# Kernel tuning notes

Hardware: AMD Instinct MI355X
Metric: run time of the kernel (lower is better)

## Reference

```python
import jax, jax.numpy as jnp
import numpy as np

TEMPERATURE = 0.5


def setup_inputs() -> dict:
    key = jax.random.key(0)
    k1, k2 = jax.random.split(key)
    N, Z = 4096, 2048
    z1 = jax.random.normal(k1, (N, Z), dtype=jnp.float32)
    z2 = jax.random.normal(k2, (N, Z), dtype=jnp.float32)
    return {"z1": z1, "z2": z2}


def reference(z1, z2):
    # NT-Xent loss. Original torch code: normalize, build full 2Nx2N cosine-sim
    # matrix, prepend the positive pair column, cross-entropy with label 0.
    # Mathematically, per-row CE with the positive prepended and the self-sim
    # removed equals: logsumexp over the row excluding the diagonal, minus the
    # positive logit.  (cosine_similarity on already-normalized vectors is a
    # plain dot product, so normalization is applied once.)
    n, _ = z1.shape
    a = z1 / jnp.linalg.norm(z1, axis=1, keepdims=True)  # [N, Z]
    b = z2 / jnp.linalg.norm(z2, axis=1, keepdims=True)  # [N, Z]
    reps = jnp.concatenate([a, b], axis=0)               # [2N, Z]
    logits = jnp.matmul(reps, reps.T) / TEMPERATURE      # [2N, 2N]
    NEG_INF = jnp.float32(-1e9)  # mask self-similarity (excluded from CE denom)
    logits = jnp.where(jnp.eye(2 * n, dtype=bool), NEG_INF, logits)
    pos = jnp.sum(a * b, axis=1) / TEMPERATURE           # [N] positive logits
    pos = jnp.concatenate([pos, pos])                    # [2N]
    lse = jax.nn.logsumexp(logits, axis=1)               # [2N]
    # sum of CE over 2N rows, divided by 2N  == mean
    return jnp.mean(lse - pos)
```

## Files before the change

kernel.cpp:

```cpp
#include <hip/hip_runtime.h>
#include <stdint.h>

#define N_ROWS 4096
#define Z_DIM  2048
#define TOT    8192
#define TILE   128
#define RBYTES (Z_DIM / 2)
#define BKE    128
#define KBYT   (BKE / 2)
#define NITER  (Z_DIM / BKE)
#define NT     (TOT / TILE)
#define NBLK   (NT * (NT + 1) / 2)
#define INV_T  2.0f
#define SCL4   64.0f

typedef __attribute__((ext_vector_type(4))) int   intx4;
typedef __attribute__((ext_vector_type(8))) int   intx8;
typedef __attribute__((ext_vector_type(4))) float floatx4;

#define GLOAD16(g, l)                                                   \
    __builtin_amdgcn_global_load_lds(                                   \
        (const __attribute__((address_space(1))) unsigned int*)(g),     \
        (__attribute__((address_space(3))) unsigned int*)(l), 16, 0, 0)

__device__ __forceinline__ unsigned int f2fp4(float v) {
    float a = fabsf(v);
    unsigned int c = (a >= 0.25f) + (a >= 0.75f) + (a >= 1.25f) + (a >= 1.75f)
                   + (a >= 2.5f)  + (a >= 3.5f)  + (a >= 5.0f);
    return c | (v < 0.f ? 8u : 0u);
}

__global__ __launch_bounds__(256) void normalize_kernel(
    const float* __restrict__ z1, const float* __restrict__ z2,
    unsigned char* __restrict__ reps, float* __restrict__ pos,
    float* __restrict__ rowsum)
{
    const int row  = blockIdx.x;
    const int tid  = threadIdx.x;
    const int lane = tid & 63, wave = tid >> 6;

    if (row < TOT / 256) rowsum[row * 256 + tid] = 0.f;

    const float4* p1 = (const float4*)(z1 + (size_t)row * Z_DIM);
    const float4* p2 = (const float4*)(z2 + (size_t)row * Z_DIM);
    float4 x0 = p1[tid * 2], x1 = p1[tid * 2 + 1];
    float4 y0 = p2[tid * 2], y1 = p2[tid * 2 + 1];

    float s1 = x0.x*x0.x + x0.y*x0.y + x0.z*x0.z + x0.w*x0.w
             + x1.x*x1.x + x1.y*x1.y + x1.z*x1.z + x1.w*x1.w;
    float s2 = y0.x*y0.x + y0.y*y0.y + y0.z*y0.z + y0.w*y0.w
             + y1.x*y1.x + y1.y*y1.y + y1.z*y1.z + y1.w*y1.w;
    float dd = x0.x*y0.x + x0.y*y0.y + x0.z*y0.z + x0.w*y0.w
             + x1.x*y1.x + x1.y*y1.y + x1.z*y1.z + x1.w*y1.w;

    #pragma unroll
    for (int m = 1; m < 64; m <<= 1) {
        s1 += __shfl_xor(s1, m);
        s2 += __shfl_xor(s2, m);
        dd += __shfl_xor(dd, m);
    }
    __shared__ float red[3][4];
    if (lane == 0) { red[0][wave] = s1; red[1][wave] = s2; red[2][wave] = dd; }
    __syncthreads();
    s1 = red[0][0] + red[0][1] + red[0][2] + red[0][3];
    s2 = red[1][0] + red[1][1] + red[1][2] + red[1][3];
    dd = red[2][0] + red[2][1] + red[2][2] + red[2][3];

    const float inv1 = rsqrtf(s1), inv2 = rsqrtf(s2);
    if (tid == 0) {
        float p = dd * inv1 * inv2 * INV_T;
        pos[row] = p;
        pos[row + N_ROWS] = p;
    }

    const float a = inv1 * SCL4, b = inv2 * SCL4;
    unsigned int pa =  f2fp4(x0.x * a)        | (f2fp4(x0.y * a) << 4)
                    | (f2fp4(x0.z * a) << 8)  | (f2fp4(x0.w * a) << 12)
                    | (f2fp4(x1.x * a) << 16) | (f2fp4(x1.y * a) << 20)
                    | (f2fp4(x1.z * a) << 24) | (f2fp4(x1.w * a) << 28);
    unsigned int pb =  f2fp4(y0.x * b)        | (f2fp4(y0.y * b) << 4)
                    | (f2fp4(y0.z * b) << 8)  | (f2fp4(y0.w * b) << 12)
                    | (f2fp4(y1.x * b) << 16) | (f2fp4(y1.y * b) << 20)
                    | (f2fp4(y1.z * b) << 24) | (f2fp4(y1.w * b) << 28);
    *(unsigned int*)(reps + (size_t)row * RBYTES + tid * 4) = pa;
    *(unsigned int*)(reps + (size_t)(N_ROWS + row) * RBYTES + tid * 4) = pb;
}

__global__ __launch_bounds__(256) void simclr_gemm(
    const unsigned char* __restrict__ reps, float* __restrict__ rowsum)
{
    __shared__ __align__(16) unsigned char L[2][2][TILE * KBYT];

    const int t = blockIdx.x;
    int r = (int)((sqrtf(8.0f * (float)t + 1.0f) - 1.0f) * 0.5f);
    while ((r + 1) * (r + 2) / 2 <= t) ++r;
    while (r * (r + 1) / 2 > t) --r;
    const int bi = t - r * (r + 1) / 2;
    const int bj = r;
    const bool diag = (bi == bj);

    const int tid  = threadIdx.x;
    const int lane = tid & 63, wave = tid >> 6;
    const int wr = wave >> 1, wc = wave & 1;
    const int quad = lane >> 4, l16 = lane & 15;
    const int sw   = l16 & 3;
    const int row0 = bi * TILE, col0 = bj * TILE;

    floatx4 acc[4][4];
    #pragma unroll
    for (int i = 0; i < 4; ++i)
        #pragma unroll
        for (int j = 0; j < 4; ++j)
            acc[i][j] = floatx4{0.f, 0.f, 0.f, 0.f};

    const int c0 = tid, c1 = tid + 256;
    const int r0s = c0 >> 2, k0s = (c0 & 3) ^ (r0s & 3);
    const int r1s = c1 >> 2, k1s = (c1 & 3) ^ (r1s & 3);
    const unsigned char* gA0 = reps + (size_t)(row0 + r0s) * RBYTES + k0s * 16;
    const unsigned char* gA1 = reps + (size_t)(row0 + r1s) * RBYTES + k1s * 16;
    const unsigned char* gB0 = reps + (size_t)(col0 + r0s) * RBYTES + k0s * 16;
    const unsigned char* gB1 = reps + (size_t)(col0 + r1s) * RBYTES + k1s * 16;
    const int o0 = c0 * 16, o1 = c1 * 16;

    GLOAD16(gA0, &L[0][0][o0]);
    GLOAD16(gA1, &L[0][0][o1]);
    GLOAD16(gB0, &L[0][1][o0]);
    GLOAD16(gB1, &L[0][1][o1]);
    __syncthreads();

    for (int i = 0; i < NITER; ++i) {
        if (i + 1 < NITER) {
            const size_t ko = (size_t)(i + 1) * KBYT;
            const int buf = (i + 1) & 1;
            GLOAD16(gA0 + ko, &L[buf][0][o0]);
            GLOAD16(gA1 + ko, &L[buf][0][o1]);
            GLOAD16(gB0 + ko, &L[buf][1][o0]);
            GLOAD16(gB1 + ko, &L[buf][1][o1]);
        }
        const unsigned char* Ab = &L[i & 1][0][0];
        const unsigned char* Bb = &L[i & 1][1][0];

        intx8 af[4], bf[4];
        #pragma unroll
        for (int fi = 0; fi < 4; ++fi) {
            const int ar = (wr * 64 + fi * 16 + l16) * KBYT;
            const int br = (wc * 64 + fi * 16 + l16) * KBYT;
            intx4 av = *(const intx4*)&Ab[ar + ((quad ^ sw) << 4)];
            intx4 bv = *(const intx4*)&Bb[br + ((quad ^ sw) << 4)];
            af[fi] = intx8{av[0], av[1], av[2], av[3], 0, 0, 0, 0};
            bf[fi] = intx8{bv[0], bv[1], bv[2], bv[3], 0, 0, 0, 0};
        }
        #pragma unroll
        for (int fi = 0; fi < 4; ++fi)
            #pragma unroll
            for (int j = 0; j < 4; ++j)
                acc[fi][j] = __builtin_amdgcn_mfma_scale_f32_16x16x128_f8f6f4(
                    af[fi], bf[j], acc[fi][j],
                    4, 4,
                    0, 0x7F7F7F7Fu,
                    0, 0x7F7F7F7Fu);
        __syncthreads();
    }

    const float descale = INV_T / (SCL4 * SCL4);
    float scol[4] = {0.f, 0.f, 0.f, 0.f};
    #pragma unroll
    for (int fi = 0; fi < 4; ++fi) {
        const int rbase = row0 + wr * 64 + fi * 16 + quad * 4;
        float srow[4] = {0.f, 0.f, 0.f, 0.f};
        #pragma unroll
        for (int j = 0; j < 4; ++j) {
            const int c = col0 + wc * 64 + j * 16 + l16;
            #pragma unroll
            for (int rr = 0; rr < 4; ++rr) {
                float e = __expf(acc[fi][j][rr] * descale);
                if (diag && (rbase + rr == c)) e = 0.f;
                srow[rr] += e;
                scol[j]  += e;
            }
        }
        #pragma unroll
        for (int rr = 0; rr < 4; ++rr) {
            #pragma unroll
            for (int m = 1; m < 16; m <<= 1) srow[rr] += __shfl_xor(srow[rr], m);
        }
        if (l16 == 0) {
            #pragma unroll
            for (int rr = 0; rr < 4; ++rr)
                atomicAdd(&rowsum[rbase + rr], srow[rr]);
        }
    }
    if (!diag) {
        #pragma unroll
        for (int j = 0; j < 4; ++j) {
            scol[j] += __shfl_xor(scol[j], 16);
            scol[j] += __shfl_xor(scol[j], 32);
        }
        if (quad == 0) {
            #pragma unroll
            for (int j = 0; j < 4; ++j)
                atomicAdd(&rowsum[col0 + wc * 64 + j * 16 + l16], scol[j]);
        }
    }
}

__global__ __launch_bounds__(1024) void finalize_kernel(
    const float* __restrict__ rowsum, const float* __restrict__ pos,
    float* __restrict__ out)
{
    const int tid = threadIdx.x;
    const int lane = tid & 63, wave = tid >> 6;
    float s = 0.f;
    for (int r = tid; r < TOT; r += 1024) s += logf(rowsum[r]) - pos[r];
    #pragma unroll
    for (int m = 1; m < 64; m <<= 1) s += __shfl_xor(s, m);
    __shared__ float red[16];
    if (lane == 0) red[wave] = s;
    __syncthreads();
    if (tid == 0) {
        float t = 0.f;
        #pragma unroll
        for (int w = 0; w < 16; ++w) t += red[w];
        out[0] = t * (1.0f / TOT);
    }
}

extern "C" void kernel_launch(void* const* d_in, const int* in_sizes, int n_in,
                              void* d_out, int out_size, void* d_ws, size_t ws_size,
                              hipStream_t stream)
{
    const float* z1 = (const float*)d_in[0];
    const float* z2 = (const float*)d_in[1];
    float* out = (float*)d_out;

    char* w = (char*)d_ws;
    unsigned char* reps = (unsigned char*)w;
    float* pos    = (float*)(w + (size_t)TOT * RBYTES);
    float* rowsum = pos + TOT;

    normalize_kernel<<<N_ROWS, 256, 0, stream>>>(z1, z2, reps, pos, rowsum);
    simclr_gemm<<<NBLK, 256, 0, stream>>>(reps, rowsum);
    finalize_kernel<<<1, 1024, 0, stream>>>(rowsum, pos, out);
}
```

Before: 155.7 us.

## Load GEMM operands directly into registers and fuse finalize via last-block reduction

The GEMM mainloop stops staging A/B tiles through LDS with global_load_lds and double buffering. Each wave now loads its own 16-byte fp4 fragments straight from global memory into registers, prefetching the next k-step, which removes the per-iteration barrier. Separately, the finalize kernel is folded into the GEMM: an atomic counter picks the last block to finish, and that block computes the logsumexp mean. This saves one launch but gives up cross-wave reuse through LDS, so global/L2 traffic and load latency rise.

```diff
diff --git a/kernel.cpp b/kernel.cpp
--- a/kernel.cpp
+++ b/kernel.cpp
@@ -18,11 +18,6 @@
 typedef __attribute__((ext_vector_type(8))) int   intx8;
 typedef __attribute__((ext_vector_type(4))) float floatx4;
 
-#define GLOAD16(g, l)                                                   \
-    __builtin_amdgcn_global_load_lds(                                   \
-        (const __attribute__((address_space(1))) unsigned int*)(g),     \
-        (__attribute__((address_space(3))) unsigned int*)(l), 16, 0, 0)
-
 __device__ __forceinline__ unsigned int f2fp4(float v) {
     float a = fabsf(v);
     unsigned int c = (a >= 0.25f) + (a >= 0.75f) + (a >= 1.25f) + (a >= 1.75f)
@@ -33,13 +28,14 @@
 __global__ __launch_bounds__(256) void normalize_kernel(
     const float* __restrict__ z1, const float* __restrict__ z2,
     unsigned char* __restrict__ reps, float* __restrict__ pos,
-    float* __restrict__ rowsum)
+    float* __restrict__ rowsum, int* __restrict__ counter)
 {
     const int row  = blockIdx.x;
     const int tid  = threadIdx.x;
     const int lane = tid & 63, wave = tid >> 6;
 
     if (row < TOT / 256) rowsum[row * 256 + tid] = 0.f;
+    if (row == 0 && tid == 0) *counter = 0;
 
     const float4* p1 = (const float4*)(z1 + (size_t)row * Z_DIM);
     const float4* p2 = (const float4*)(z2 + (size_t)row * Z_DIM);
@@ -87,10 +83,10 @@
 }
 
 __global__ __launch_bounds__(256) void simclr_gemm(
-    const unsigned char* __restrict__ reps, float* __restrict__ rowsum)
+    const unsigned char* __restrict__ reps, float* __restrict__ rowsum,
+    const float* __restrict__ pos, int* __restrict__ counter,
+    float* __restrict__ out)
 {
-    __shared__ __align__(16) unsigned char L[2][2][TILE * KBYT];
-
     const int t = blockIdx.x;
     int r = (int)((sqrtf(8.0f * (float)t + 1.0f) - 1.0f) * 0.5f);
     while ((r + 1) * (r + 2) / 2 <= t) ++r;
@@ -103,8 +99,12 @@
     const int lane = tid & 63, wave = tid >> 6;
     const int wr = wave >> 1, wc = wave & 1;
     const int quad = lane >> 4, l16 = lane & 15;
-    const int sw   = l16 & 3;
     const int row0 = bi * TILE, col0 = bj * TILE;
+
+    const unsigned char* Abase =
+        reps + (size_t)(row0 + wr * 64 + l16) * RBYTES + quad * 16;
+    const unsigned char* Bbase =
+        reps + (size_t)(col0 + wc * 64 + l16) * RBYTES + quad * 16;
 
     floatx4 acc[4][4];
     #pragma unroll
@@ -113,53 +113,41 @@
         for (int j = 0; j < 4; ++j)
             acc[i][j] = floatx4{0.f, 0.f, 0.f, 0.f};
 
-    const int c0 = tid, c1 = tid + 256;
-    const int r0s = c0 >> 2, k0s = (c0 & 3) ^ (r0s & 3);
-    const int r1s = c1 >> 2, k1s = (c1 & 3) ^ (r1s & 3);
-    const unsigned char* gA0 = reps + (size_t)(row0 + r0s) * RBYTES + k0s * 16;
-    const unsigned char* gA1 = reps + (size_t)(row0 + r1s) * RBYTES + k1s * 16;
-    const unsigned char* gB0 = reps + (size_t)(col0 + r0s) * RBYTES + k0s * 16;
-    const unsigned char* gB1 = reps + (size_t)(col0 + r1s) * RBYTES + k1s * 16;
-    const int o0 = c0 * 16, o1 = c1 * 16;
-
-    GLOAD16(gA0, &L[0][0][o0]);
-    GLOAD16(gA1, &L[0][0][o1]);
-    GLOAD16(gB0, &L[0][1][o0]);
-    GLOAD16(gB1, &L[0][1][o1]);
-    __syncthreads();
-
+    intx4 a_cur[4], b_cur[4];
+    #pragma unroll
+    for (int f = 0; f < 4; ++f) {
+        a_cur[f] = *(const intx4*)(Abase + (size_t)f * 16 * RBYTES);
+        b_cur[f] = *(const intx4*)(Bbase + (size_t)f * 16 * RBYTES);
+    }
+
+    #pragma unroll 2
     for (int i = 0; i < NITER; ++i) {
+        intx4 a_nxt[4], b_nxt[4];
         if (i + 1 < NITER) {
             const size_t ko = (size_t)(i + 1) * KBYT;
-            const int buf = (i + 1) & 1;
-            GLOAD16(gA0 + ko, &L[buf][0][o0]);
-            GLOAD16(gA1 + ko, &L[buf][0][o1]);
-            GLOAD16(gB0 + ko, &L[buf][1][o0]);
-            GLOAD16(gB1 + ko, &L[buf][1][o1]);
-        }
-        const unsigned char* Ab = &L[i & 1][0][0];
-        const unsigned char* Bb = &L[i & 1][1][0];
-
-        intx8 af[4], bf[4];
+            #pragma unroll
+            for (int f = 0; f < 4; ++f) {
+                a_nxt[f] = *(const intx4*)(Abase + ko + (size_t)f * 16 * RBYTES);
+                b_nxt[f] = *(const intx4*)(Bbase + ko + (size_t)f * 16 * RBYTES);
+            }
+        }
         #pragma unroll
         for (int fi = 0; fi < 4; ++fi) {
-            const int ar = (wr * 64 + fi * 16 + l16) * KBYT;
-            const int br = (wc * 64 + fi * 16 + l16) * KBYT;
-            intx4 av = *(const intx4*)&Ab[ar + ((quad ^ sw) << 4)];
-            intx4 bv = *(const intx4*)&Bb[br + ((quad ^ sw) << 4)];
-            af[fi] = intx8{av[0], av[1], av[2], av[3], 0, 0, 0, 0};
-            bf[fi] = intx8{bv[0], bv[1], bv[2], bv[3], 0, 0, 0, 0};
-        }
-        #pragma unroll
-        for (int fi = 0; fi < 4; ++fi)
-            #pragma unroll
-            for (int j = 0; j < 4; ++j)
+            intx8 aop = intx8{a_cur[fi][0], a_cur[fi][1], a_cur[fi][2], a_cur[fi][3],
+                              0, 0, 0, 0};
+            #pragma unroll
+            for (int j = 0; j < 4; ++j) {
+                intx8 bop = intx8{b_cur[j][0], b_cur[j][1], b_cur[j][2], b_cur[j][3],
+                                  0, 0, 0, 0};
                 acc[fi][j] = __builtin_amdgcn_mfma_scale_f32_16x16x128_f8f6f4(
-                    af[fi], bf[j], acc[fi][j],
+                    aop, bop, acc[fi][j],
                     4, 4,
                     0, 0x7F7F7F7Fu,
                     0, 0x7F7F7F7Fu);
-        __syncthreads();
+            }
+        }
+        #pragma unroll
+        for (int f = 0; f < 4; ++f) { a_cur[f] = a_nxt[f]; b_cur[f] = b_nxt[f]; }
     }
 
     const float descale = INV_T / (SCL4 * SCL4);
@@ -202,26 +190,24 @@
                 atomicAdd(&rowsum[col0 + wc * 64 + j * 16 + l16], scol[j]);
         }
     }
-}
-
-__global__ __launch_bounds__(1024) void finalize_kernel(
-    const float* __restrict__ rowsum, const float* __restrict__ pos,
-    float* __restrict__ out)
-{
-    const int tid = threadIdx.x;
-    const int lane = tid & 63, wave = tid >> 6;
-    float s = 0.f;
-    for (int r = tid; r < TOT; r += 1024) s += logf(rowsum[r]) - pos[r];
-    #pragma unroll
-    for (int m = 1; m < 64; m <<= 1) s += __shfl_xor(s, m);
-    __shared__ float red[16];
-    if (lane == 0) red[wave] = s;
+
     __syncthreads();
-    if (tid == 0) {
-        float t = 0.f;
-        #pragma unroll
-        for (int w = 0; w < 16; ++w) t += red[w];
-        out[0] = t * (1.0f / TOT);
+    __threadfence();
+    __shared__ int lastBlock;
+    __shared__ float red[4];
+    if (tid == 0) lastBlock = (atomicAdd(counter, 1) == NBLK - 1) ? 1 : 0;
+    __syncthreads();
+    if (lastBlock) {
+        float s = 0.f;
+        for (int rr = tid; rr < TOT; rr += 256) {
+            float rs = atomicAdd(&rowsum[rr], 0.0f);
+            s += logf(rs) - pos[rr];
+        }
+        #pragma unroll
+        for (int m = 1; m < 64; m <<= 1) s += __shfl_xor(s, m);
+        if (lane == 0) red[wave] = s;
+        __syncthreads();
+        if (tid == 0) out[0] = (red[0] + red[1] + red[2] + red[3]) * (1.0f / TOT);
     }
 }
 
@@ -237,8 +223,8 @@
     unsigned char* reps = (unsigned char*)w;
     float* pos    = (float*)(w + (size_t)TOT * RBYTES);
     float* rowsum = pos + TOT;
-
-    normalize_kernel<<<N_ROWS, 256, 0, stream>>>(z1, z2, reps, pos, rowsum);
-    simclr_gemm<<<NBLK, 256, 0, stream>>>(reps, rowsum);
-    finalize_kernel<<<1, 1024, 0, stream>>>(rowsum, pos, out);
-}
+    int*   counter = (int*)(rowsum + TOT);
+
+    normalize_kernel<<<N_ROWS, 256, 0, stream>>>(z1, z2, reps, pos, rowsum, counter);
+    simclr_gemm<<<NBLK, 256, 0, stream>>>(reps, rowsum, pos, counter, out);
+}
```

Result: slower. 416.3 us (+167.4%).
